# Performance work log

Hardware: AMD Instinct MI355X
Metric: run time of the kernel (lower is better)

## Reference

```python
import jax, jax.numpy as jnp
import numpy as np

ALPHA = 0.01  # leaky_relu slope (forward default)

def _hist_entropy(x, bins):
    """Mean over batch of per-sample histogram entropy, matching
    np.histogram(sample, bins=bins) + entropy_calc(hist, bw=bins):
      H = -sum(p*log(p)) - log(1/bins) = -sum(p*log(p)) + log(bins).
    x: [B, D] float."""
    B, D = x.shape
    xmin = jnp.min(x, axis=1, keepdims=True)
    xmax = jnp.max(x, axis=1, keepdims=True)
    width = xmax - xmin
    safe_w = jnp.where(width > 0, width, 1.0)
    # np.histogram: equal-width bins over [min, max]; max value goes in last bin
    idx = jnp.floor((x - xmin) / safe_w * bins).astype(jnp.int32)
    idx = jnp.clip(idx, 0, bins - 1)
    flat = (jnp.arange(B, dtype=jnp.int32)[:, None] * bins + idx).reshape(-1)
    counts = jnp.zeros(B * bins, jnp.float32).at[flat].add(1.0).reshape(B, bins)
    p = counts / jnp.float32(D)
    plogp = jnp.where(p > 0, p * jnp.log(jnp.where(p > 0, p, 1.0)), 0.0)
    H = -jnp.sum(plogp, axis=1) + jnp.log(jnp.float32(bins))  # [B]
    return jnp.mean(H)

def _lin(x, W, b):
    return x @ W.T + b

def setup_inputs() -> dict:
    key = jax.random.key(0)
    ks = jax.random.split(key, 13)
    B = 65536
    dims = [(784, 256), (256, 128), (128, 128), (128, 128), (128, 32), (32, 10)]
    inp = {"x": jax.random.normal(ks[0], (B, 784), dtype=jnp.float32)}
    for i, (din, dout) in enumerate(dims):
        s = 1.0 / np.sqrt(din)
        inp[f"W{i+1}"] = jax.random.uniform(ks[1 + 2 * i], (dout, din), jnp.float32, -s, s)
        inp[f"b{i+1}"] = jax.random.uniform(ks[2 + 2 * i], (dout,), jnp.float32, -s, s)
    return inp

def reference(x, W1, b1, W2, b2, W3, b3, W4, b4, W5, b5, W6, b6):
    x = x.reshape(-1, 784)
    Hs = []
    for (W, b) in [(W1, b1), (W2, b2), (W3, b3), (W4, b4), (W5, b5)]:
        x = jax.nn.leaky_relu(_lin(x, W, b), ALPHA)
        Hs.append(_hist_entropy(x, x.shape[1]))  # bins = dim / bin_ratio(=1)
    x = jax.nn.relu(_lin(x, W6, b6))
    out = jax.nn.log_softmax(x, axis=1)
    return (out, Hs[0], Hs[1], Hs[2], Hs[3], Hs[4])
```

## Files before the change

### kernel.cpp

```cpp
#include <hip/hip_runtime.h>
#include <hip/hip_bf16.h>
#include <math.h>

#define ALPHA 0.01f

typedef __bf16 bf16x8 __attribute__((ext_vector_type(8)));
typedef float  floatx4 __attribute__((ext_vector_type(4)));

static __device__ __forceinline__ unsigned short f2bf_bits(float f) {
    return __builtin_bit_cast(unsigned short, (__bf16)f);
}
static __device__ __forceinline__ float bf2f(unsigned short u) {
    return __builtin_bit_cast(float, (unsigned)u << 16);
}

static __device__ __forceinline__ void glds16(const void* g, void* l) {
    __builtin_amdgcn_global_load_lds(
        (const __attribute__((address_space(1))) unsigned int*)g,
        (__attribute__((address_space(3))) unsigned int*)l, 16, 0, 0);
}

template <int CTRL>
static __device__ __forceinline__ float dppmov(float x) {
    int r = __builtin_amdgcn_update_dpp(0, __builtin_bit_cast(int, x), CTRL, 0xf, 0xf, false);
    return __builtin_bit_cast(float, r);
}
static __device__ __forceinline__ float red16min(float x) {
    x = fminf(x, dppmov<0x121>(x)); x = fminf(x, dppmov<0x122>(x));
    x = fminf(x, dppmov<0x124>(x)); x = fminf(x, dppmov<0x128>(x));
    return x;
}
static __device__ __forceinline__ float red16max(float x) {
    x = fmaxf(x, dppmov<0x121>(x)); x = fmaxf(x, dppmov<0x122>(x));
    x = fmaxf(x, dppmov<0x124>(x)); x = fmaxf(x, dppmov<0x128>(x));
    return x;
}
static __device__ __forceinline__ float red16sum(float x) {
    x += dppmov<0x121>(x); x += dppmov<0x122>(x);
    x += dppmov<0x124>(x); x += dppmov<0x128>(x);
    return x;
}

template <int DIN, int DOUT, bool XF32, bool WRES, int MINB>
__global__ __launch_bounds__(256, MINB) void layer_mfma(
    const void* __restrict__ Xin, const unsigned short* __restrict__ Wf,
    const float* __restrict__ bias, unsigned short* __restrict__ Y,
    float* __restrict__ Hpart)
{
    constexpr int CTN     = DOUT / 16;
    constexpr int KT_FULL = DIN / 32;
    constexpr int TAIL    = DIN % 32;
    constexpr int HALF    = DOUT / 2;
    constexpr int LOG2D   = (DOUT == 256) ? 8 : (DOUT == 128) ? 7 : 5;
    constexpr float LOGB  = (DOUT == 256) ? 5.54517744f
                          : (DOUT == 128) ? 4.85203026f : 3.46573590f;
    constexpr int XBYTES  = WRES ? 16 : 64 * 32 * (XF32 ? 4 : 2);
    constexpr int WBYTES  = WRES ? (size_t)DIN * DOUT * 2 : DOUT * 64;
    constexpr int WSLOTS  = (DIN / 32) * CTN * 64;
    static_assert(DOUT % 32 == 0 && DOUT <= 256, "DOUT");
    static_assert(XF32 || TAIL == 0, "bf16 input requires DIN%32==0");

    __shared__ __align__(16) char smemX[XBYTES];
    __shared__ __align__(16) char smemW[WBYTES];
    __shared__ unsigned int counts[16][HALF + 1];
    __shared__ float hsum[4];

    const int t      = threadIdx.x;
    const int lane   = t & 63;
    const int lane16 = lane & 15;
    const int q      = lane >> 4;
    const int w      = t >> 6;
    const int row0   = blockIdx.x * 64;
    const int myrow  = w * 16 + lane16;

    float biasr[CTN];
    #pragma unroll
    for (int ct = 0; ct < CTN; ct++) biasr[ct] = bias[ct * 16 + lane16];

    floatx4 acc[CTN];
    #pragma unroll
    for (int ct = 0; ct < CTN; ct++) acc[ct] = (floatx4)(0.0f);

    if constexpr (WRES) {
        static_assert(WSLOTS % 256 == 0, "WSLOTS");
        #pragma unroll
        for (int i = 0; i < WSLOTS / 256; i++)
            glds16(Wf + ((size_t)(i * 256 + w * 64 + lane)) * 8,
                   smemW + (i * 256 + w * 64) * 16);
        __syncthreads();

        const unsigned short* X = (const unsigned short*)Xin;
        const size_t abase = (size_t)(row0 + myrow) * DIN + q * 8;
        bf16x8 acur = *(const bf16x8*)(X + abase);
        #pragma unroll
        for (int kt = 0; kt < KT_FULL; kt++) {
            bf16x8 anxt = acur;
            if (kt + 1 < KT_FULL)
                anxt = *(const bf16x8*)(X + abase + (kt + 1) * 32);
            #pragma unroll
            for (int ct = 0; ct < CTN; ct++) {
                bf16x8 bw = *(const bf16x8*)(smemW + ((kt * CTN + ct) * 64 + lane) * 16);
                acc[ct] = __builtin_amdgcn_mfma_f32_16x16x32_bf16(acur, bw, acc[ct], 0, 0, 0);
            }
            acur = anxt;
        }
    } else {
        auto stageW = [&](int kt) {
            #pragma unroll
            for (int j = w; j < CTN; j += 4)
                glds16(Wf + ((size_t)kt * CTN * 64 + j * 64 + lane) * 8,
                       smemW + j * 64 * 16);
        };
        auto stageX = [&](int kt) {
            const float* X = (const float*)Xin;
            #pragma unroll
            for (int j = 0; j < 2; j++) {
                int s  = w * 128 + j * 64 + lane;
                int gc = (s & ~7) | ((s ^ (s >> 3)) & 7);
                int r  = gc >> 3, c = gc & 7;
                glds16(X + (size_t)(row0 + r) * DIN + kt * 32 + c * 4,
                       smemX + (w * 128 + j * 64) * 16);
            }
        };
        auto compute = [&]() {
            int s0 = myrow * 8 + (((2 * q)     ^ myrow) & 7);
            int s1 = myrow * 8 + (((2 * q + 1) ^ myrow) & 7);
            float4 f0 = *(const float4*)(smemX + s0 * 16);
            float4 f1 = *(const float4*)(smemX + s1 * 16);
            uint4 pk;
            pk.x = (unsigned)f2bf_bits(f0.x) | ((unsigned)f2bf_bits(f0.y) << 16);
            pk.y = (unsigned)f2bf_bits(f0.z) | ((unsigned)f2bf_bits(f0.w) << 16);
            pk.z = (unsigned)f2bf_bits(f1.x) | ((unsigned)f2bf_bits(f1.y) << 16);
            pk.w = (unsigned)f2bf_bits(f1.z) | ((unsigned)f2bf_bits(f1.w) << 16);
            bf16x8 a = __builtin_bit_cast(bf16x8, pk);
            #pragma unroll
            for (int ct = 0; ct < CTN; ct++) {
                bf16x8 bw = *(const bf16x8*)(smemW + (ct * 64 + lane) * 16);
                acc[ct] = __builtin_amdgcn_mfma_f32_16x16x32_bf16(a, bw, acc[ct], 0, 0, 0);
            }
        };

        #pragma unroll 1
        for (int kt = 0; kt < KT_FULL; kt++) {
            __syncthreads();
            stageX(kt);
            stageW(kt);
            __syncthreads();
            compute();
        }
        if constexpr (TAIL > 0) {
            __syncthreads();
            stageW(KT_FULL);
            {
                const float* X = (const float*)Xin;
                int r = t >> 2, c = t & 3;
                float4 v = *(const float4*)(X + (size_t)(row0 + r) * DIN
                                            + KT_FULL * 32 + c * 4);
                *(float4*)(smemX + (r * 8 + ((c ^ r) & 7)) * 16) = v;
                int c2 = c + 4;
                *(float4*)(smemX + (r * 8 + ((c2 ^ r) & 7)) * 16)
                    = make_float4(0.f, 0.f, 0.f, 0.f);
            }
            __syncthreads();
            compute();
        }
    }

    #pragma unroll
    for (int ct = 0; ct < CTN; ct++) {
        #pragma unroll
        for (int reg = 0; reg < 4; reg++) {
            float v = acc[ct][reg] + biasr[ct];
            v = v > 0.0f ? v : ALPHA * v;
            acc[ct][reg] = v;
            Y[(size_t)(row0 + w * 16 + q * 4 + reg) * DOUT
              + ct * 16 + lane16] = f2bf_bits(v);
        }
    }

    unsigned int* cc = counts[w * 4 + q];
    float Hq = 0.0f;
    #pragma unroll
    for (int reg = 0; reg < 4; reg++) {
        float mn = acc[0][reg], mx = mn;
        #pragma unroll
        for (int ct = 1; ct < CTN; ct++) {
            mn = fminf(mn, acc[ct][reg]);
            mx = fmaxf(mx, acc[ct][reg]);
        }
        mn = red16min(mn);
        mx = red16max(mx);
        float wdt = mx - mn;
        float scale = (float)DOUT / (wdt > 0.0f ? wdt : 1.0f);

        #pragma unroll
        for (int i = 0; i < DOUT / 32; i++) cc[lane16 + 16 * i] = 0u;

        #pragma unroll
        for (int ct = 0; ct < CTN; ct++) {
            int b = (int)((acc[ct][reg] - mn) * scale);
            b = b < (DOUT - 1) ? b : (DOUT - 1);
            atomicAdd(&cc[b & (HALF - 1)],
                      1u << (((b >> (LOG2D - 1)) & 1) << 4));
        }

        float s = 0.0f;
        #pragma unroll
        for (int i = 0; i < DOUT / 32; i++) {
            unsigned int word = cc[lane16 + 16 * i];
            int c0 = (int)(word & 0xffffu), c1 = (int)(word >> 16);
            if (c0 > 0) { float p = (float)c0 * (1.0f / (float)DOUT); s += p * __logf(p); }
            if (c1 > 0) { float p = (float)c1 * (1.0f / (float)DOUT); s += p * __logf(p); }
        }
        s = red16sum(s);
        Hq += LOGB - s;
    }
    Hq += __shfl_xor(Hq, 16, 64);
    Hq += __shfl_xor(Hq, 32, 64);

    if (lane == 0) hsum[w] = Hq;
    __syncthreads();
    if (t == 0) Hpart[blockIdx.x] = hsum[0] + hsum[1] + hsum[2] + hsum[3];
}

__global__ void convert_wfrag(const float* __restrict__ W1, const float* __restrict__ W2,
                              const float* __restrict__ W3, const float* __restrict__ W4,
                              const float* __restrict__ W5, unsigned short* __restrict__ out)
{
    int s = blockIdx.x * 256 + threadIdx.x;
    if (s >= 34304) return;
    const float* W; int DIN, CTN, sl;
    if      (s < 25600) { W = W1; DIN = 784; CTN = 16; sl = s;         }
    else if (s < 29696) { W = W2; DIN = 256; CTN = 8;  sl = s - 25600; }
    else if (s < 31744) { W = W3; DIN = 128; CTN = 8;  sl = s - 29696; }
    else if (s < 33792) { W = W4; DIN = 128; CTN = 8;  sl = s - 31744; }
    else                { W = W5; DIN = 128; CTN = 2;  sl = s - 33792; }
    int kt = sl / (CTN * 64);
    int ct = (sl / 64) % CTN;
    int ln = sl & 63;
    int r  = ct * 16 + (ln & 15);
    int k0 = kt * 32 + (ln >> 4) * 8;
    unsigned short v[8];
    #pragma unroll
    for (int j = 0; j < 8; j++) {
        int k = k0 + j;
        v[j] = (k < DIN) ? f2bf_bits(W[(size_t)r * DIN + k]) : (unsigned short)0;
    }
    uint4 pk;
    pk.x = (unsigned)v[0] | ((unsigned)v[1] << 16);
    pk.y = (unsigned)v[2] | ((unsigned)v[3] << 16);
    pk.z = (unsigned)v[4] | ((unsigned)v[5] << 16);
    pk.w = (unsigned)v[6] | ((unsigned)v[7] << 16);
    *(uint4*)(out + (size_t)s * 8) = pk;
}

__global__ __launch_bounds__(256) void layer6_kernel(
    const unsigned short* __restrict__ Xb, const float* __restrict__ W,
    const float* __restrict__ b, float* __restrict__ out,
    const float* __restrict__ Hpart, float* __restrict__ out_tail)
{
    __shared__ float Wl[320];
    __shared__ float bl[10];
    __shared__ float hred[4][5];
    const int t = threadIdx.x;
    const int lane = t & 63;
    const int w = t >> 6;

    if (blockIdx.x == 0) {
        #pragma unroll
        for (int l = 0; l < 5; l++) {
            float s = Hpart[l * 1024 + t]       + Hpart[l * 1024 + t + 256]
                    + Hpart[l * 1024 + t + 512] + Hpart[l * 1024 + t + 768];
            #pragma unroll
            for (int off = 1; off <= 32; off <<= 1) s += __shfl_xor(s, off, 64);
            if (lane == 0) hred[w][l] = s;
        }
        __syncthreads();
        if (t < 5)
            out_tail[t] = (hred[0][t] + hred[1][t] + hred[2][t] + hred[3][t])
                          * (1.0f / 65536.0f);
    }

    for (int i = t; i < 320; i += 256) Wl[i] = W[i];
    if (t < 10) bl[t] = b[t];
    __syncthreads();

    const size_t row = (size_t)blockIdx.x * 256 + t;
    float x[32];
    const uint4* xp = (const uint4*)(Xb + row * 32);
    #pragma unroll
    for (int i = 0; i < 4; i++) {
        uint4 v = xp[i];
        unsigned u[4] = {v.x, v.y, v.z, v.w};
        #pragma unroll
        for (int j = 0; j < 4; j++) {
            x[8 * i + 2 * j]     = bf2f((unsigned short)(u[j] & 0xffffu));
            x[8 * i + 2 * j + 1] = bf2f((unsigned short)(u[j] >> 16));
        }
    }

    float z[10];
    float m = -1e30f;
    #pragma unroll
    for (int j = 0; j < 10; j++) {
        float s = bl[j];
        #pragma unroll
        for (int k = 0; k < 32; k++) s = fmaf(x[k], Wl[j * 32 + k], s);
        z[j] = fmaxf(s, 0.0f);
        m = fmaxf(m, z[j]);
    }
    float se = 0.0f;
    #pragma unroll
    for (int j = 0; j < 10; j++) se += __expf(z[j] - m);
    float ls = __logf(se);
    float* op = out + row * 10;
    #pragma unroll
    for (int j = 0; j < 10; j++) op[j] = z[j] - m - ls;
}

extern "C" void kernel_launch(void* const* d_in, const int* in_sizes, int n_in,
                              void* d_out, int out_size, void* d_ws, size_t ws_size,
                              hipStream_t stream)
{
    const float* x  = (const float*)d_in[0];
    const float* W1 = (const float*)d_in[1];  const float* b1 = (const float*)d_in[2];
    const float* W2 = (const float*)d_in[3];  const float* b2 = (const float*)d_in[4];
    const float* W3 = (const float*)d_in[5];  const float* b3 = (const float*)d_in[6];
    const float* W4 = (const float*)d_in[7];  const float* b4 = (const float*)d_in[8];
    const float* W5 = (const float*)d_in[9];  const float* b5 = (const float*)d_in[10];
    const float* W6 = (const float*)d_in[11]; const float* b6 = (const float*)d_in[12];
    float* out = (float*)d_out;

    constexpr int B = 65536;
    char* ws = (char*)d_ws;
    float* Hpart = (float*)ws;
    unsigned short* Wfrag = (unsigned short*)(ws + 20480);
    unsigned short* W1f = Wfrag;
    unsigned short* W2f = W1f + 25600 * 8;
    unsigned short* W3f = W2f + 4096 * 8;
    unsigned short* W4f = W3f + 2048 * 8;
    unsigned short* W5f = W4f + 2048 * 8;
    unsigned short* bufA = (unsigned short*)(ws + (1 << 20));
    unsigned short* bufB = (unsigned short*)(ws + (1 << 20) + (size_t)B * 512);

    convert_wfrag<<<134, 256, 0, stream>>>(W1, W2, W3, W4, W5, Wfrag);

    layer_mfma<784, 256, true , false, 4><<<B / 64, 256, 0, stream>>>(x,    W1f, b1, bufA, Hpart + 0 * 1024);
    layer_mfma<256, 128, false, true , 2><<<B / 64, 256, 0, stream>>>(bufA, W2f, b2, bufB, Hpart + 1 * 1024);
    layer_mfma<128, 128, false, true , 4><<<B / 64, 256, 0, stream>>>(bufB, W3f, b3, bufA, Hpart + 2 * 1024);
    layer_mfma<128, 128, false, true , 4><<<B / 64, 256, 0, stream>>>(bufA, W4f, b4, bufB, Hpart + 3 * 1024);
    layer_mfma<128,  32, false, true , 4><<<B / 64, 256, 0, stream>>>(bufB, W5f, b5, bufA, Hpart + 4 * 1024);

    layer6_kernel<<<B / 256, 256, 0, stream>>>(bufA, W6, b6, out, Hpart, out + (size_t)B * 10);
}
```

Before: 410.2 us.

## Fuse layers 2-6 into one per-wave kernel keeping activations in LDS

Replaces the four separate layer_mfma launches for layers 2-5 and the layer6 kernel with a single tail_fused kernel. Each wave processes 16 rows through layers 2 to 6, keeping the intermediate bf16 activations in a swizzled LDS tile instead of writing them to global buffers and reading them back. The histogram-entropy partials are now written per wave, and a small hreduce kernel sums them at the end. This removes several kernel launches and the global-memory round trips of the intermediates. In exchange the fused kernel is bound to 3 blocks per SM, has higher register and LDS pressure, and gives up per-layer tuning.

```diff
diff --git a/kernel.cpp b/kernel.cpp
--- a/kernel.cpp
+++ b/kernel.cpp
@@ -9,9 +9,6 @@
 
 static __device__ __forceinline__ unsigned short f2bf_bits(float f) {
     return __builtin_bit_cast(unsigned short, (__bf16)f);
-}
-static __device__ __forceinline__ float bf2f(unsigned short u) {
-    return __builtin_bit_cast(float, (unsigned)u << 16);
 }
 
 static __device__ __forceinline__ void glds16(const void* g, void* l) {
@@ -223,6 +220,179 @@
     if (t == 0) Hpart[blockIdx.x] = hsum[0] + hsum[1] + hsum[2] + hsum[3];
 }
 
+template <int DIN, int DOUT, bool AG>
+static __device__ __forceinline__ float tail_layer(
+    const unsigned short* __restrict__ Ag, size_t arow,
+    char* __restrict__ yt,
+    const unsigned short* __restrict__ Wf, const float* __restrict__ bias,
+    unsigned int* __restrict__ cc, int lane)
+{
+    constexpr int KT  = DIN / 32, CTN = DOUT / 16;
+    constexpr int NCI = DIN / 8,  NCO = DOUT / 8;
+    constexpr int HALF  = DOUT / 2;
+    constexpr int LOG2D = (DOUT == 128) ? 7 : 5;
+    constexpr float LOGB = (DOUT == 128) ? 4.85203026f : 3.46573590f;
+    const int lane16 = lane & 15, q = lane >> 4;
+
+    bf16x8 a[KT];
+    if constexpr (AG) {
+        #pragma unroll
+        for (int kt = 0; kt < KT; kt++)
+            a[kt] = *(const bf16x8*)(Ag + arow + q * 8 + kt * 32);
+    } else {
+        asm volatile("s_waitcnt lgkmcnt(0)" ::: "memory");
+        #pragma unroll
+        for (int kt = 0; kt < KT; kt++) {
+            int cs = (kt * 4 + q) ^ (lane16 & (NCI - 1));
+            a[kt] = *(const bf16x8*)(yt + lane16 * (DIN * 2) + cs * 16);
+        }
+    }
+
+    float biasr[CTN];
+    #pragma unroll
+    for (int ct = 0; ct < CTN; ct++) biasr[ct] = bias[ct * 16 + lane16];
+
+    floatx4 acc[CTN];
+    #pragma unroll
+    for (int ct = 0; ct < CTN; ct++) acc[ct] = (floatx4)(0.0f);
+
+    #pragma unroll
+    for (int kt = 0; kt < KT; kt++) {
+        #pragma unroll
+        for (int ct = 0; ct < CTN; ct++) {
+            bf16x8 bw = *(const bf16x8*)(Wf + ((size_t)(kt * CTN + ct) * 64 + lane) * 8);
+            acc[ct] = __builtin_amdgcn_mfma_f32_16x16x32_bf16(a[kt], bw, acc[ct], 0, 0, 0);
+        }
+    }
+
+    #pragma unroll
+    for (int ct = 0; ct < CTN; ct++) {
+        #pragma unroll
+        for (int reg = 0; reg < 4; reg++) {
+            float v = acc[ct][reg] + biasr[ct];
+            v = v > 0.0f ? v : ALPHA * v;
+            acc[ct][reg] = v;
+            int r  = q * 4 + reg;
+            int c  = (ct * 16 + lane16) >> 3;
+            int cs = c ^ (r & (NCO - 1));
+            *(unsigned short*)(yt + r * (DOUT * 2) + cs * 16 + (lane16 & 7) * 2)
+                = f2bf_bits(v);
+        }
+    }
+
+    float Hq = 0.0f;
+    #pragma unroll
+    for (int reg = 0; reg < 4; reg++) {
+        float mn = acc[0][reg], mx = mn;
+        #pragma unroll
+        for (int ct = 1; ct < CTN; ct++) {
+            mn = fminf(mn, acc[ct][reg]);
+            mx = fmaxf(mx, acc[ct][reg]);
+        }
+        mn = red16min(mn);
+        mx = red16max(mx);
+        float wdt = mx - mn;
+        float scale = (float)DOUT / (wdt > 0.0f ? wdt : 1.0f);
+
+        #pragma unroll
+        for (int i = 0; i < DOUT / 32; i++) cc[lane16 + 16 * i] = 0u;
+
+        #pragma unroll
+        for (int ct = 0; ct < CTN; ct++) {
+            int b = (int)((acc[ct][reg] - mn) * scale);
+            b = b < (DOUT - 1) ? b : (DOUT - 1);
+            atomicAdd(&cc[b & (HALF - 1)],
+                      1u << (((b >> (LOG2D - 1)) & 1) << 4));
+        }
+
+        float s = 0.0f;
+        #pragma unroll
+        for (int i = 0; i < DOUT / 32; i++) {
+            unsigned int word = cc[lane16 + 16 * i];
+            int c0 = (int)(word & 0xffffu), c1 = (int)(word >> 16);
+            if (c0 > 0) { float p = (float)c0 * (1.0f / (float)DOUT); s += p * __logf(p); }
+            if (c1 > 0) { float p = (float)c1 * (1.0f / (float)DOUT); s += p * __logf(p); }
+        }
+        s = red16sum(s);
+        Hq += LOGB - s;
+    }
+    Hq += __shfl_xor(Hq, 16, 64);
+    Hq += __shfl_xor(Hq, 32, 64);
+    return Hq;
+}
+
+__global__ __launch_bounds__(256, 3) void tail_fused(
+    const unsigned short* __restrict__ Xb,
+    const unsigned short* __restrict__ W2f, const float* __restrict__ b2,
+    const unsigned short* __restrict__ W3f, const float* __restrict__ b3,
+    const unsigned short* __restrict__ W4f, const float* __restrict__ b4,
+    const unsigned short* __restrict__ W5f, const float* __restrict__ b5,
+    const float* __restrict__ W6, const float* __restrict__ b6,
+    float* __restrict__ out, float* __restrict__ Hpart)
+{
+    __shared__ __align__(16) char yts[4][16 * 128 * 2];
+    __shared__ unsigned int counts[16][65];
+
+    const int t = threadIdx.x;
+    const int lane = t & 63, lane16 = lane & 15, q = lane >> 4, w = t >> 6;
+    char* yt = yts[w];
+    unsigned int* cc = counts[w * 4 + q];
+    const int row0 = blockIdx.x * 64 + w * 16;
+    const size_t arow = (size_t)(row0 + lane16) * 256;
+    const int hidx = blockIdx.x * 4 + w;
+
+    float H;
+    H = tail_layer<256, 128, true >(Xb, arow, yt, W2f, b2, cc, lane);
+    if (lane == 0) Hpart[1 * 4096 + hidx] = H;
+    H = tail_layer<128, 128, false>(Xb, 0, yt, W3f, b3, cc, lane);
+    if (lane == 0) Hpart[2 * 4096 + hidx] = H;
+    H = tail_layer<128, 128, false>(Xb, 0, yt, W4f, b4, cc, lane);
+    if (lane == 0) Hpart[3 * 4096 + hidx] = H;
+    H = tail_layer<128,  32, false>(Xb, 0, yt, W5f, b5, cc, lane);
+    if (lane == 0) Hpart[4 * 4096 + hidx] = H;
+
+    asm volatile("s_waitcnt lgkmcnt(0)" ::: "memory");
+    float x[32];
+    #pragma unroll
+    for (int c = 0; c < 4; c++) {
+        int cs = c ^ (lane16 & 3);
+        bf16x8 v = *(const bf16x8*)(yt + lane16 * 64 + cs * 16);
+        #pragma unroll
+        for (int j = 0; j < 8; j++) x[c * 8 + j] = (float)v[j];
+    }
+
+    float z[3];
+    float m = -1e30f;
+    #pragma unroll
+    for (int s2 = 0; s2 < 3; s2++) {
+        int jj = q * 3 + s2;
+        float a6 = 0.0f;
+        if (jj < 10) {
+            a6 = b6[jj];
+            #pragma unroll
+            for (int k = 0; k < 32; k++) a6 = fmaf(x[k], W6[jj * 32 + k], a6);
+            a6 = fmaxf(a6, 0.0f);
+            m = fmaxf(m, a6);
+        }
+        z[s2] = a6;
+    }
+    m = fmaxf(m, __shfl_xor(m, 16, 64));
+    m = fmaxf(m, __shfl_xor(m, 32, 64));
+    float se = 0.0f;
+    #pragma unroll
+    for (int s2 = 0; s2 < 3; s2++)
+        if (q * 3 + s2 < 10) se += __expf(z[s2] - m);
+    se += __shfl_xor(se, 16, 64);
+    se += __shfl_xor(se, 32, 64);
+    float ls = __logf(se);
+    const size_t ro = (size_t)(row0 + lane16) * 10;
+    #pragma unroll
+    for (int s2 = 0; s2 < 3; s2++) {
+        int jj = q * 3 + s2;
+        if (jj < 10) out[ro + jj] = z[s2] - m - ls;
+    }
+}
+
 __global__ void convert_wfrag(const float* __restrict__ W1, const float* __restrict__ W2,
                               const float* __restrict__ W3, const float* __restrict__ W4,
                               const float* __restrict__ W5, unsigned short* __restrict__ out)
@@ -254,68 +424,22 @@
     *(uint4*)(out + (size_t)s * 8) = pk;
 }
 
-__global__ __launch_bounds__(256) void layer6_kernel(
-    const unsigned short* __restrict__ Xb, const float* __restrict__ W,
-    const float* __restrict__ b, float* __restrict__ out,
-    const float* __restrict__ Hpart, float* __restrict__ out_tail)
-{
-    __shared__ float Wl[320];
-    __shared__ float bl[10];
-    __shared__ float hred[4][5];
-    const int t = threadIdx.x;
-    const int lane = t & 63;
-    const int w = t >> 6;
-
-    if (blockIdx.x == 0) {
-        #pragma unroll
-        for (int l = 0; l < 5; l++) {
-            float s = Hpart[l * 1024 + t]       + Hpart[l * 1024 + t + 256]
-                    + Hpart[l * 1024 + t + 512] + Hpart[l * 1024 + t + 768];
-            #pragma unroll
-            for (int off = 1; off <= 32; off <<= 1) s += __shfl_xor(s, off, 64);
-            if (lane == 0) hred[w][l] = s;
-        }
-        __syncthreads();
-        if (t < 5)
-            out_tail[t] = (hred[0][t] + hred[1][t] + hred[2][t] + hred[3][t])
-                          * (1.0f / 65536.0f);
-    }
-
-    for (int i = t; i < 320; i += 256) Wl[i] = W[i];
-    if (t < 10) bl[t] = b[t];
+__global__ __launch_bounds__(256) void hreduce(const float* __restrict__ Hp,
+                                               float* __restrict__ out_tail)
+{
+    __shared__ float sm[4];
+    const int t = threadIdx.x, lane = t & 63, w = t >> 6;
+    const int l = blockIdx.x;
+    const int n = l ? 4096 : 1024;
+    const float* p = Hp + (size_t)l * 4096;
+    float s = 0.0f;
+    for (int i = t; i < n; i += 256) s += p[i];
+    #pragma unroll
+    for (int off = 1; off <= 32; off <<= 1) s += __shfl_xor(s, off, 64);
+    if (lane == 0) sm[w] = s;
     __syncthreads();
-
-    const size_t row = (size_t)blockIdx.x * 256 + t;
-    float x[32];
-    const uint4* xp = (const uint4*)(Xb + row * 32);
-    #pragma unroll
-    for (int i = 0; i < 4; i++) {
-        uint4 v = xp[i];
-        unsigned u[4] = {v.x, v.y, v.z, v.w};
-        #pragma unroll
-        for (int j = 0; j < 4; j++) {
-            x[8 * i + 2 * j]     = bf2f((unsigned short)(u[j] & 0xffffu));
-            x[8 * i + 2 * j + 1] = bf2f((unsigned short)(u[j] >> 16));
-        }
-    }
-
-    float z[10];
-    float m = -1e30f;
-    #pragma unroll
-    for (int j = 0; j < 10; j++) {
-        float s = bl[j];
-        #pragma unroll
-        for (int k = 0; k < 32; k++) s = fmaf(x[k], Wl[j * 32 + k], s);
-        z[j] = fmaxf(s, 0.0f);
-        m = fmaxf(m, z[j]);
-    }
-    float se = 0.0f;
-    #pragma unroll
-    for (int j = 0; j < 10; j++) se += __expf(z[j] - m);
-    float ls = __logf(se);
-    float* op = out + row * 10;
-    #pragma unroll
-    for (int j = 0; j < 10; j++) op[j] = z[j] - m - ls;
+    if (t == 0)
+        out_tail[l] = (sm[0] + sm[1] + sm[2] + sm[3]) * (1.0f / 65536.0f);
 }
 
 extern "C" void kernel_launch(void* const* d_in, const int* in_sizes, int n_in,
@@ -334,22 +458,21 @@
     constexpr int B = 65536;
     char* ws = (char*)d_ws;
     float* Hpart = (float*)ws;
-    unsigned short* Wfrag = (unsigned short*)(ws + 20480);
+    unsigned short* Wfrag = (unsigned short*)(ws + 81920);
     unsigned short* W1f = Wfrag;
     unsigned short* W2f = W1f + 25600 * 8;
     unsigned short* W3f = W2f + 4096 * 8;
     unsigned short* W4f = W3f + 2048 * 8;
     unsigned short* W5f = W4f + 2048 * 8;
     unsigned short* bufA = (unsigned short*)(ws + (1 << 20));
-    unsigned short* bufB = (unsigned short*)(ws + (1 << 20) + (size_t)B * 512);
 
     convert_wfrag<<<134, 256, 0, stream>>>(W1, W2, W3, W4, W5, Wfrag);
 
-    layer_mfma<784, 256, true , false, 4><<<B / 64, 256, 0, stream>>>(x,    W1f, b1, bufA, Hpart + 0 * 1024);
-    layer_mfma<256, 128, false, true , 2><<<B / 64, 256, 0, stream>>>(bufA, W2f, b2, bufB, Hpart + 1 * 1024);
-    layer_mfma<128, 128, false, true , 4><<<B / 64, 256, 0, stream>>>(bufB, W3f, b3, bufA, Hpart + 2 * 1024);
-    layer_mfma<128, 128, false, true , 4><<<B / 64, 256, 0, stream>>>(bufA, W4f, b4, bufB, Hpart + 3 * 1024);
-    layer_mfma<128,  32, false, true , 4><<<B / 64, 256, 0, stream>>>(bufB, W5f, b5, bufA, Hpart + 4 * 1024);
-
-    layer6_kernel<<<B / 256, 256, 0, stream>>>(bufA, W6, b6, out, Hpart, out + (size_t)B * 10);
-}
+    layer_mfma<784, 256, true, false, 4><<<B / 64, 256, 0, stream>>>(
+        x, W1f, b1, bufA, Hpart);
+
+    tail_fused<<<B / 64, 256, 0, stream>>>(
+        bufA, W2f, b2, W3f, b3, W4f, b4, W5f, b5, W6, b6, out, Hpart);
+
+    hreduce<<<5, 256, 0, stream>>>(Hpart, out + (size_t)B * 10);
+}
```

Result: no change. 408.4 us (-0.4%).
